# Optimization experiments

Measured on AMD Instinct MI355X. Metric: run time of the kernel, lower is better.

The kernel has to match this reference:

```python
import jax, jax.numpy as jnp
import numpy as np

B, IN, OUT = 131072, 256, 256
BITWIDTH = 7.0


def setup_inputs() -> dict:
    key = jax.random.key(0)
    k1, k2 = jax.random.split(key)
    # simulated int8 activations (integer-valued float32)
    act_in = jax.random.randint(k1, (B, IN), -127, 128).astype(jnp.float32)
    # UniformWeights: xavier_uniform then weight_quant to the int8 grid
    limit = float(np.sqrt(6.0 / (IN + OUT)))
    w = jax.random.uniform(k2, (OUT, IN), minval=-limit, maxval=limit, dtype=jnp.float32)
    w_range = jnp.max(jnp.abs(w))
    weight_exp = (jnp.ceil(jnp.log2(w_range)) - 7.0).astype(jnp.int32)
    weight = jnp.round(w / w_range * 127.0)  # int8-valued float32 [OUT, IN]
    return {"act_in": act_in, "exp_in": jnp.int32(0), "weight": weight, "weight_exp": weight_exp}


def _round_shift(x, shift):
    # RoundShift: floor-div by 2**shift, add floor(|remainder| / 2**(shift-1)), clip to int8
    two_s = jnp.exp2(shift)
    rt = jnp.floor(x / two_s)
    prob = jnp.abs(x - rt * two_s)
    dec = jnp.floor(prob / jnp.exp2(shift - 1.0))
    return jnp.clip(rt + dec, -127.0, 127.0)


def reference(act_in, exp_in, weight, weight_exp):
    # int8 GEMM simulated in fp32 (exact: |acc| < 2^24)
    temp = act_in @ weight.T  # [B, OUT] int32 accumulator values
    # RangeEstimate: full-tensor abs-max -> bitwidth
    r = jnp.max(jnp.abs(temp))
    bw = jnp.where(r > 0, jnp.ceil(jnp.log2(jnp.maximum(r, 1.0))), 0.0)
    shift = bw - BITWIDTH
    pos = shift > 0
    safe_shift = jnp.maximum(shift, 1.0)
    rounded = _round_shift(temp, safe_shift)
    act_out = jnp.where(pos, rounded, temp).astype(jnp.int8)
    exp_sum = jnp.asarray(exp_in, jnp.int32) + jnp.asarray(weight_exp, jnp.int32)
    exp_out = (exp_sum + jnp.where(pos, shift, 0.0).astype(jnp.int32)).astype(jnp.int16)
    return act_out, exp_out
```

## Files before the change

### kernel.cpp

```cpp
#include <hip/hip_runtime.h>
#include <stdint.h>


#define M_ROWS 131072
#define NK 256
#define BM 64
#define BK 64
#define BKP 72

typedef __attribute__((ext_vector_type(8))) short bf16x8;
typedef __attribute__((ext_vector_type(4))) float f32x4;
typedef __attribute__((ext_vector_type(4))) float fv4;
typedef __attribute__((ext_vector_type(4))) int iv4;
typedef __attribute__((ext_vector_type(4))) unsigned int u32x4;
typedef __attribute__((ext_vector_type(4))) unsigned short us4;

__device__ __forceinline__ uint32_t pack_bf16(float a, float b) {
  return (__float_as_uint(a) >> 16) | (__float_as_uint(b) & 0xFFFF0000u);
}

__global__ void wconv(const float* __restrict__ w, unsigned short* __restrict__ wb) {
  const int i = blockIdx.x * 256 + threadIdx.x;
  const fv4 f = ((const fv4*)w)[i];
  us4 o;
  o.x = (unsigned short)(__float_as_uint(f.x) >> 16);
  o.y = (unsigned short)(__float_as_uint(f.y) >> 16);
  o.z = (unsigned short)(__float_as_uint(f.z) >> 16);
  o.w = (unsigned short)(__float_as_uint(f.w) >> 16);
  ((us4*)wb)[i] = o;
}

__global__ __launch_bounds__(256, 3) void gemm_pass1(
    const float* __restrict__ act,
    const unsigned short* __restrict__ wgtb,
    int* __restrict__ temp,
    int* __restrict__ gmax)
{
  __shared__ __align__(16) short As[BM * BKP];
  __shared__ __align__(16) short Bs[NK * BKP];
  __shared__ int smax;

  const int tid = threadIdx.x;
  if (tid == 0) smax = 0;

  const int bm   = blockIdx.x * BM;
  const int lane = tid & 63;
  const int wave = tid >> 6;
  const int lm   = lane & 15;
  const int lk   = lane >> 4;
  const int wn   = wave * 64;

  const int arow = tid >> 3, aks = (tid & 7) * 8;
  const int brow = tid >> 3, bks = (tid & 7) * 8;

  uint32_t apk[2][4];
  u32x4 breg[8];

#pragma unroll
  for (int j = 0; j < 2; ++j) {
    const float* p = act + (size_t)(bm + arow + j * 32) * NK + aks;
    const fv4 f0 = __builtin_nontemporal_load((const fv4*)p);
    const fv4 f1 = __builtin_nontemporal_load((const fv4*)p + 1);
    apk[j][0] = pack_bf16(f0.x, f0.y); apk[j][1] = pack_bf16(f0.z, f0.w);
    apk[j][2] = pack_bf16(f1.x, f1.y); apk[j][3] = pack_bf16(f1.z, f1.w);
  }
#pragma unroll
  for (int j = 0; j < 8; ++j)
    breg[j] = *(const u32x4*)(wgtb + (size_t)(brow + j * 32) * NK + bks);

  f32x4 acc[4][4] = {};

  for (int kt = 0; kt < NK; kt += BK) {
    __syncthreads();
#pragma unroll
    for (int j = 0; j < 2; ++j)
      *(u32x4*)&As[(arow + j * 32) * BKP + aks] = *(const u32x4*)apk[j];
#pragma unroll
    for (int j = 0; j < 8; ++j)
      *(u32x4*)&Bs[(brow + j * 32) * BKP + bks] = breg[j];
    __syncthreads();

    if (kt + BK < NK) {
      const int ktn = kt + BK;
#pragma unroll
      for (int j = 0; j < 2; ++j) {
        const float* p = act + (size_t)(bm + arow + j * 32) * NK + ktn + aks;
        const fv4 f0 = __builtin_nontemporal_load((const fv4*)p);
        const fv4 f1 = __builtin_nontemporal_load((const fv4*)p + 1);
        apk[j][0] = pack_bf16(f0.x, f0.y); apk[j][1] = pack_bf16(f0.z, f0.w);
        apk[j][2] = pack_bf16(f1.x, f1.y); apk[j][3] = pack_bf16(f1.z, f1.w);
      }
#pragma unroll
      for (int j = 0; j < 8; ++j)
        breg[j] = *(const u32x4*)(wgtb + (size_t)(brow + j * 32) * NK + ktn + bks);
    }

#pragma unroll
    for (int kk = 0; kk < BK; kk += 32) {
      bf16x8 af[4], bfr[4];
#pragma unroll
      for (int mi = 0; mi < 4; ++mi)
        af[mi] = *(const bf16x8*)&As[(mi * 16 + lm) * BKP + kk + lk * 8];
#pragma unroll
      for (int ni = 0; ni < 4; ++ni)
        bfr[ni] = *(const bf16x8*)&Bs[(wn + ni * 16 + lm) * BKP + kk + lk * 8];
#pragma unroll
      for (int mi = 0; mi < 4; ++mi)
#pragma unroll
        for (int ni = 0; ni < 4; ++ni)
          acc[mi][ni] = __builtin_amdgcn_mfma_f32_16x16x32_bf16(
              af[mi], bfr[ni], acc[mi][ni], 0, 0, 0);
    }
  }

  int imax = 0;
#pragma unroll
  for (int mi = 0; mi < 4; ++mi)
#pragma unroll
    for (int ni = 0; ni < 4; ++ni)
#pragma unroll
      for (int r = 0; r < 4; ++r) {
        const float v = acc[mi][ni][r];
        const int iv = (int)v;
        const int m = bm + mi * 16 + lk * 4 + r;
        const int n = wn + ni * 16 + lm;
        __builtin_nontemporal_store(iv, &temp[(size_t)m * NK + n]);
        const int a = iv < 0 ? -iv : iv;
        imax = a > imax ? a : imax;
      }
#pragma unroll
  for (int off = 32; off; off >>= 1) {
    const int o = __shfl_xor(imax, off, 64);
    imax = o > imax ? o : imax;
  }
  if (lane == 0) atomicMax(&smax, imax);
  __syncthreads();
  if (tid == 0) atomicMax(gmax, smax);
}

__global__ void quant_pass2(int* __restrict__ temp,
                            const int* __restrict__ gmax,
                            const int* __restrict__ exp_in,
                            const int* __restrict__ wexp)
{
  const int r = *gmax;
  const int bw = (r <= 1) ? 0 : (32 - __clz(r - 1));
  const int shift = bw - 7;
  const bool pos = shift > 0;
  const int s = shift < 1 ? 1 : shift;

  const int total4 = (M_ROWS * NK) / 4;
  iv4* p = (iv4*)temp;
  const int idx = blockIdx.x * blockDim.x + threadIdx.x;
  const int stride = gridDim.x * blockDim.x;

  for (int i = idx; i < total4; i += stride) {
    const iv4 t = __builtin_nontemporal_load(&p[i]);
    iv4 o;
#pragma unroll
    for (int j = 0; j < 4; ++j) {
      const int ti = t[j];
      int q;
      if (pos) {
        const int rt = ti >> s;
        const int dec = (ti - (rt << s)) >> (s - 1);
        q = rt + dec;
        q = q > 127 ? 127 : (q < -127 ? -127 : q);
      } else {
        q = (int)(signed char)(ti & 0xFF);
      }
      o[j] = q;
    }
    __builtin_nontemporal_store(o, &p[i]);
  }

  if (idx == 0) {
    const int e = exp_in[0] + wexp[0] + (pos ? shift : 0);
    temp[(size_t)M_ROWS * NK] = (int)(short)e;
  }
}

extern "C" void kernel_launch(void* const* d_in, const int* in_sizes, int n_in,
                              void* d_out, int out_size, void* d_ws, size_t ws_size,
                              hipStream_t stream) {
  const float* act   = (const float*)d_in[0];
  const int* exp_in  = (const int*)d_in[1];
  const float* wgt   = (const float*)d_in[2];
  const int* wexp    = (const int*)d_in[3];
  int* gmax          = (int*)d_ws;
  unsigned short* wb = (unsigned short*)((char*)d_ws + 128);

  (void)hipMemsetAsync(d_ws, 0, sizeof(int), stream);
  wconv<<<dim3(64), dim3(256), 0, stream>>>(wgt, wb);
  gemm_pass1<<<dim3(M_ROWS / BM), dim3(256), 0, stream>>>(act, wb, (int*)d_out, gmax);
  quant_pass2<<<dim3(4096), dim3(256), 0, stream>>>((int*)d_out, gmax, exp_in, wexp);
}
```

Before: 303.2 us.

## Recompute GEMM in quant pass instead of storing and reloading int32 accumulators

Splits the work into a GEMM pass that only computes the global abs-max and a second GEMM pass that recomputes the tile and quantizes it directly in registers before storing. This removes the round trip of writing the full int32 temp tensor and reading it back in a separate quantize kernel. In exchange, the activations are read twice and the matrix multiply is done twice. Activation loads also switch from nontemporal to regular loads.

```diff
diff --git a/kernel.cpp b/kernel.cpp
--- a/kernel.cpp
+++ b/kernel.cpp
@@ -30,19 +30,11 @@
   ((us4*)wb)[i] = o;
 }
 
-__global__ __launch_bounds__(256, 3) void gemm_pass1(
-    const float* __restrict__ act,
-    const unsigned short* __restrict__ wgtb,
-    int* __restrict__ temp,
-    int* __restrict__ gmax)
+__device__ __forceinline__ void gemm_tile(
+    const float* __restrict__ act, const unsigned short* __restrict__ wgtb,
+    short* As, short* Bs, f32x4 acc[4][4])
 {
-  __shared__ __align__(16) short As[BM * BKP];
-  __shared__ __align__(16) short Bs[NK * BKP];
-  __shared__ int smax;
-
-  const int tid = threadIdx.x;
-  if (tid == 0) smax = 0;
-
+  const int tid  = threadIdx.x;
   const int bm   = blockIdx.x * BM;
   const int lane = tid & 63;
   const int wave = tid >> 6;
@@ -59,16 +51,14 @@
 #pragma unroll
   for (int j = 0; j < 2; ++j) {
     const float* p = act + (size_t)(bm + arow + j * 32) * NK + aks;
-    const fv4 f0 = __builtin_nontemporal_load((const fv4*)p);
-    const fv4 f1 = __builtin_nontemporal_load((const fv4*)p + 1);
+    const fv4 f0 = *(const fv4*)p;
+    const fv4 f1 = *((const fv4*)p + 1);
     apk[j][0] = pack_bf16(f0.x, f0.y); apk[j][1] = pack_bf16(f0.z, f0.w);
     apk[j][2] = pack_bf16(f1.x, f1.y); apk[j][3] = pack_bf16(f1.z, f1.w);
   }
 #pragma unroll
   for (int j = 0; j < 8; ++j)
     breg[j] = *(const u32x4*)(wgtb + (size_t)(brow + j * 32) * NK + bks);
-
-  f32x4 acc[4][4] = {};
 
   for (int kt = 0; kt < NK; kt += BK) {
     __syncthreads();
@@ -85,8 +75,8 @@
 #pragma unroll
       for (int j = 0; j < 2; ++j) {
         const float* p = act + (size_t)(bm + arow + j * 32) * NK + ktn + aks;
-        const fv4 f0 = __builtin_nontemporal_load((const fv4*)p);
-        const fv4 f1 = __builtin_nontemporal_load((const fv4*)p + 1);
+        const fv4 f0 = *(const fv4*)p;
+        const fv4 f1 = *((const fv4*)p + 1);
         apk[j][0] = pack_bf16(f0.x, f0.y); apk[j][1] = pack_bf16(f0.z, f0.w);
         apk[j][2] = pack_bf16(f1.x, f1.y); apk[j][3] = pack_bf16(f1.z, f1.w);
       }
@@ -112,6 +102,20 @@
               af[mi], bfr[ni], acc[mi][ni], 0, 0, 0);
     }
   }
+}
+
+__global__ __launch_bounds__(256, 3) void gemm_max(
+    const float* __restrict__ act, const unsigned short* __restrict__ wgtb,
+    int* __restrict__ gmax)
+{
+  __shared__ __align__(16) short As[BM * BKP];
+  __shared__ __align__(16) short Bs[NK * BKP];
+  __shared__ int smax;
+  const int tid = threadIdx.x;
+  if (tid == 0) smax = 0;
+
+  f32x4 acc[4][4] = {};
+  gemm_tile(act, wgtb, As, Bs, acc);
 
   int imax = 0;
 #pragma unroll
@@ -120,11 +124,7 @@
     for (int ni = 0; ni < 4; ++ni)
 #pragma unroll
       for (int r = 0; r < 4; ++r) {
-        const float v = acc[mi][ni][r];
-        const int iv = (int)v;
-        const int m = bm + mi * 16 + lk * 4 + r;
-        const int n = wn + ni * 16 + lm;
-        __builtin_nontemporal_store(iv, &temp[(size_t)m * NK + n]);
+        const int iv = (int)acc[mi][ni][r];
         const int a = iv < 0 ? -iv : iv;
         imax = a > imax ? a : imax;
       }
@@ -133,50 +133,59 @@
     const int o = __shfl_xor(imax, off, 64);
     imax = o > imax ? o : imax;
   }
-  if (lane == 0) atomicMax(&smax, imax);
+  if ((tid & 63) == 0) atomicMax(&smax, imax);
   __syncthreads();
   if (tid == 0) atomicMax(gmax, smax);
 }
 
-__global__ void quant_pass2(int* __restrict__ temp,
-                            const int* __restrict__ gmax,
-                            const int* __restrict__ exp_in,
-                            const int* __restrict__ wexp)
+__global__ __launch_bounds__(256, 3) void gemm_quant(
+    const float* __restrict__ act, const unsigned short* __restrict__ wgtb,
+    int* __restrict__ out, const int* __restrict__ gmax,
+    const int* __restrict__ exp_in, const int* __restrict__ wexp)
 {
-  const int r = *gmax;
-  const int bw = (r <= 1) ? 0 : (32 - __clz(r - 1));
+  __shared__ __align__(16) short As[BM * BKP];
+  __shared__ __align__(16) short Bs[NK * BKP];
+
+  const int rmax = *gmax;
+  const int bw = (rmax <= 1) ? 0 : (32 - __clz(rmax - 1));
   const int shift = bw - 7;
   const bool pos = shift > 0;
   const int s = shift < 1 ? 1 : shift;
 
-  const int total4 = (M_ROWS * NK) / 4;
-  iv4* p = (iv4*)temp;
-  const int idx = blockIdx.x * blockDim.x + threadIdx.x;
-  const int stride = gridDim.x * blockDim.x;
-
-  for (int i = idx; i < total4; i += stride) {
-    const iv4 t = __builtin_nontemporal_load(&p[i]);
-    iv4 o;
-#pragma unroll
-    for (int j = 0; j < 4; ++j) {
-      const int ti = t[j];
-      int q;
-      if (pos) {
-        const int rt = ti >> s;
-        const int dec = (ti - (rt << s)) >> (s - 1);
-        q = rt + dec;
-        q = q > 127 ? 127 : (q < -127 ? -127 : q);
-      } else {
-        q = (int)(signed char)(ti & 0xFF);
+  f32x4 acc[4][4] = {};
+  gemm_tile(act, wgtb, As, Bs, acc);
+
+  const int tid  = threadIdx.x;
+  const int bm   = blockIdx.x * BM;
+  const int lane = tid & 63;
+  const int lm   = lane & 15;
+  const int lk   = lane >> 4;
+  const int wn   = (tid >> 6) * 64;
+
+#pragma unroll
+  for (int mi = 0; mi < 4; ++mi)
+#pragma unroll
+    for (int ni = 0; ni < 4; ++ni)
+#pragma unroll
+      for (int r = 0; r < 4; ++r) {
+        const int ti = (int)acc[mi][ni][r];
+        int q;
+        if (pos) {
+          const int rt = ti >> s;
+          const int dec = (ti - (rt << s)) >> (s - 1);
+          q = rt + dec;
+          q = q > 127 ? 127 : (q < -127 ? -127 : q);
+        } else {
+          q = (int)(signed char)(ti & 0xFF);
+        }
+        const int m = bm + mi * 16 + lk * 4 + r;
+        const int n = wn + ni * 16 + lm;
+        __builtin_nontemporal_store(q, &out[(size_t)m * NK + n]);
       }
-      o[j] = q;
-    }
-    __builtin_nontemporal_store(o, &p[i]);
-  }
-
-  if (idx == 0) {
+
+  if (blockIdx.x == 0 && tid == 0) {
     const int e = exp_in[0] + wexp[0] + (pos ? shift : 0);
-    temp[(size_t)M_ROWS * NK] = (int)(short)e;
+    out[(size_t)M_ROWS * NK] = (int)(short)e;
   }
 }
 
@@ -192,6 +201,7 @@
 
   (void)hipMemsetAsync(d_ws, 0, sizeof(int), stream);
   wconv<<<dim3(64), dim3(256), 0, stream>>>(wgt, wb);
-  gemm_pass1<<<dim3(M_ROWS / BM), dim3(256), 0, stream>>>(act, wb, (int*)d_out, gmax);
-  quant_pass2<<<dim3(4096), dim3(256), 0, stream>>>((int*)d_out, gmax, exp_in, wexp);
-}
+  gemm_max<<<dim3(M_ROWS / BM), dim3(256), 0, stream>>>(act, wb, gmax);
+  gemm_quant<<<dim3(M_ROWS / BM), dim3(256), 0, stream>>>(act, wb, (int*)d_out,
+                                                          gmax, exp_in, wexp);
+}
```

New measurement: 281.4 us. 7.2% less time.

## Stage full-K activation tile in LDS, read weights from global, use separate temp buffer

Applied to the files above, without the earlier changes.

The GEMM kernel now loads the whole 64x256 activation tile into LDS once and reads bf16 weight fragments straight from global memory (which stays L2-resident), removing the K-loop double buffer, the weight LDS tile and the per-step barriers. The intermediate int32 accumulator is written with cached stores to a separate workspace buffer instead of the output, and the quantize pass reads it with normal loads, so the 128MB temp may partly hit the cache. In exchange, every wave issues repeated global weight loads, and the removed occupancy hint plus the larger LDS footprint may change occupancy.

```diff
diff --git a/kernel.cpp b/kernel.cpp
--- a/kernel.cpp
+++ b/kernel.cpp
@@ -5,8 +5,7 @@
 #define M_ROWS 131072
 #define NK 256
 #define BM 64
-#define BK 64
-#define BKP 72
+#define AKP 264
 
 typedef __attribute__((ext_vector_type(8))) short bf16x8;
 typedef __attribute__((ext_vector_type(4))) float f32x4;
@@ -30,14 +29,13 @@
   ((us4*)wb)[i] = o;
 }
 
-__global__ __launch_bounds__(256, 3) void gemm_pass1(
+__global__ __launch_bounds__(256) void gemm_store_max(
     const float* __restrict__ act,
     const unsigned short* __restrict__ wgtb,
     int* __restrict__ temp,
     int* __restrict__ gmax)
 {
-  __shared__ __align__(16) short As[BM * BKP];
-  __shared__ __align__(16) short Bs[NK * BKP];
+  __shared__ __align__(16) short As[BM * AKP];
   __shared__ int smax;
 
   const int tid = threadIdx.x;
@@ -50,67 +48,43 @@
   const int lk   = lane >> 4;
   const int wn   = wave * 64;
 
-  const int arow = tid >> 3, aks = (tid & 7) * 8;
-  const int brow = tid >> 3, bks = (tid & 7) * 8;
-
-  uint32_t apk[2][4];
-  u32x4 breg[8];
-
+  {
+    const int arow = tid >> 5;
+    const int aseg = tid & 31;
+    const float* pbase = act + (size_t)(bm + arow) * NK + aseg * 8;
 #pragma unroll
-  for (int j = 0; j < 2; ++j) {
-    const float* p = act + (size_t)(bm + arow + j * 32) * NK + aks;
-    const fv4 f0 = __builtin_nontemporal_load((const fv4*)p);
-    const fv4 f1 = __builtin_nontemporal_load((const fv4*)p + 1);
-    apk[j][0] = pack_bf16(f0.x, f0.y); apk[j][1] = pack_bf16(f0.z, f0.w);
-    apk[j][2] = pack_bf16(f1.x, f1.y); apk[j][3] = pack_bf16(f1.z, f1.w);
+    for (int j = 0; j < 8; ++j) {
+      const float* p = pbase + (size_t)(j * 8) * NK;
+      const fv4 f0 = *(const fv4*)p;
+      const fv4 f1 = *((const fv4*)p + 1);
+      uint32_t pk[4];
+      pk[0] = pack_bf16(f0.x, f0.y); pk[1] = pack_bf16(f0.z, f0.w);
+      pk[2] = pack_bf16(f1.x, f1.y); pk[3] = pack_bf16(f1.z, f1.w);
+      *(u32x4*)&As[(arow + j * 8) * AKP + aseg * 8] = *(const u32x4*)pk;
+    }
   }
-#pragma unroll
-  for (int j = 0; j < 8; ++j)
-    breg[j] = *(const u32x4*)(wgtb + (size_t)(brow + j * 32) * NK + bks);
+  __syncthreads();
 
   f32x4 acc[4][4] = {};
 
-  for (int kt = 0; kt < NK; kt += BK) {
-    __syncthreads();
+  const unsigned short* bbase = wgtb + (size_t)(wn + lm) * NK + lk * 8;
 #pragma unroll
-    for (int j = 0; j < 2; ++j)
-      *(u32x4*)&As[(arow + j * 32) * BKP + aks] = *(const u32x4*)apk[j];
+  for (int k8 = 0; k8 < 8; ++k8) {
+    const int kk = k8 * 32;
+    bf16x8 af[4];
+    u32x4 bf[4];
 #pragma unroll
-    for (int j = 0; j < 8; ++j)
-      *(u32x4*)&Bs[(brow + j * 32) * BKP + bks] = breg[j];
-    __syncthreads();
-
-    if (kt + BK < NK) {
-      const int ktn = kt + BK;
+    for (int ni = 0; ni < 4; ++ni)
+      bf[ni] = *(const u32x4*)(bbase + (size_t)(ni * 16) * NK + kk);
 #pragma unroll
-      for (int j = 0; j < 2; ++j) {
-        const float* p = act + (size_t)(bm + arow + j * 32) * NK + ktn + aks;
-        const fv4 f0 = __builtin_nontemporal_load((const fv4*)p);
-        const fv4 f1 = __builtin_nontemporal_load((const fv4*)p + 1);
-        apk[j][0] = pack_bf16(f0.x, f0.y); apk[j][1] = pack_bf16(f0.z, f0.w);
-        apk[j][2] = pack_bf16(f1.x, f1.y); apk[j][3] = pack_bf16(f1.z, f1.w);
-      }
+    for (int mi = 0; mi < 4; ++mi)
+      af[mi] = *(const bf16x8*)&As[(mi * 16 + lm) * AKP + kk + lk * 8];
 #pragma unroll
-      for (int j = 0; j < 8; ++j)
-        breg[j] = *(const u32x4*)(wgtb + (size_t)(brow + j * 32) * NK + ktn + bks);
-    }
-
-#pragma unroll
-    for (int kk = 0; kk < BK; kk += 32) {
-      bf16x8 af[4], bfr[4];
-#pragma unroll
-      for (int mi = 0; mi < 4; ++mi)
-        af[mi] = *(const bf16x8*)&As[(mi * 16 + lm) * BKP + kk + lk * 8];
+    for (int mi = 0; mi < 4; ++mi)
 #pragma unroll
       for (int ni = 0; ni < 4; ++ni)
-        bfr[ni] = *(const bf16x8*)&Bs[(wn + ni * 16 + lm) * BKP + kk + lk * 8];
-#pragma unroll
-      for (int mi = 0; mi < 4; ++mi)
-#pragma unroll
-        for (int ni = 0; ni < 4; ++ni)
-          acc[mi][ni] = __builtin_amdgcn_mfma_f32_16x16x32_bf16(
-              af[mi], bfr[ni], acc[mi][ni], 0, 0, 0);
-    }
+        acc[mi][ni] = __builtin_amdgcn_mfma_f32_16x16x32_bf16(
+            af[mi], *(const bf16x8*)&bf[ni], acc[mi][ni], 0, 0, 0);
   }
 
   int imax = 0;
@@ -120,11 +94,10 @@
     for (int ni = 0; ni < 4; ++ni)
 #pragma unroll
       for (int r = 0; r < 4; ++r) {
-        const float v = acc[mi][ni][r];
-        const int iv = (int)v;
+        const int iv = (int)acc[mi][ni][r];
         const int m = bm + mi * 16 + lk * 4 + r;
         const int n = wn + ni * 16 + lm;
-        __builtin_nontemporal_store(iv, &temp[(size_t)m * NK + n]);
+        temp[(size_t)m * NK + n] = iv;
         const int a = iv < 0 ? -iv : iv;
         imax = a > imax ? a : imax;
       }
@@ -138,10 +111,10 @@
   if (tid == 0) atomicMax(gmax, smax);
 }
 
-__global__ void quant_pass2(int* __restrict__ temp,
-                            const int* __restrict__ gmax,
-                            const int* __restrict__ exp_in,
-                            const int* __restrict__ wexp)
+__global__ __launch_bounds__(256) void quant_stream(
+    const int* __restrict__ temp, int* __restrict__ out,
+    const int* __restrict__ gmax,
+    const int* __restrict__ exp_in, const int* __restrict__ wexp)
 {
   const int r = *gmax;
   const int bw = (r <= 1) ? 0 : (32 - __clz(r - 1));
@@ -150,12 +123,13 @@
   const int s = shift < 1 ? 1 : shift;
 
   const int total4 = (M_ROWS * NK) / 4;
-  iv4* p = (iv4*)temp;
+  const iv4* pin = (const iv4*)temp;
+  iv4* pout = (iv4*)out;
   const int idx = blockIdx.x * blockDim.x + threadIdx.x;
   const int stride = gridDim.x * blockDim.x;
 
   for (int i = idx; i < total4; i += stride) {
-    const iv4 t = __builtin_nontemporal_load(&p[i]);
+    const iv4 t = pin[i];
     iv4 o;
 #pragma unroll
     for (int j = 0; j < 4; ++j) {
@@ -171,12 +145,12 @@
       }
       o[j] = q;
     }
-    __builtin_nontemporal_store(o, &p[i]);
+    __builtin_nontemporal_store(o, &pout[i]);
   }
 
   if (idx == 0) {
     const int e = exp_in[0] + wexp[0] + (pos ? shift : 0);
-    temp[(size_t)M_ROWS * NK] = (int)(short)e;
+    out[(size_t)M_ROWS * NK] = (int)(short)e;
   }
 }
 
@@ -187,11 +161,14 @@
   const int* exp_in  = (const int*)d_in[1];
   const float* wgt   = (const float*)d_in[2];
   const int* wexp    = (const int*)d_in[3];
+
   int* gmax          = (int*)d_ws;
-  unsigned short* wb = (unsigned short*)((char*)d_ws + 128);
+  unsigned short* wb = (unsigned short*)((char*)d_ws + 4096);
+  int* temp          = (int*)((char*)d_ws + (1 << 20));
 
   (void)hipMemsetAsync(d_ws, 0, sizeof(int), stream);
   wconv<<<dim3(64), dim3(256), 0, stream>>>(wgt, wb);
-  gemm_pass1<<<dim3(M_ROWS / BM), dim3(256), 0, stream>>>(act, wb, (int*)d_out, gmax);
-  quant_pass2<<<dim3(4096), dim3(256), 0, stream>>>((int*)d_out, gmax, exp_in, wexp);
+  gemm_store_max<<<dim3(M_ROWS / BM), dim3(256), 0, stream>>>(act, wb, temp, gmax);
+  quant_stream<<<dim3(4096), dim3(256), 0, stream>>>(temp, (int*)d_out, gmax,
+                                                     exp_in, wexp);
 }
```

Measured after the change: 304.5 us. About the same (+0.4%).
